# Performance work log

Measured on AMD Instinct MI355X. Metric: run time of the kernel, lower is better.

Reference implementation:

```python
import jax, jax.numpy as jnp
import numpy as np

B, N, S, H = 128, 512, 8, 64
HORIZON = 12


def setup_inputs() -> dict:
    key = jax.random.key(0)
    ks = jax.random.split(key, 24)
    sc = 0.05
    inp = {
        "crowd_obsv": jax.random.normal(ks[0], (B, N, S, 2), jnp.float32),
        "pad_mask": jax.random.bernoulli(ks[1], 0.9, (B, N, N)),
        "neg_hist_mask": jnp.ones((B, N, S, 1), jnp.float32),
        # LSTM params (PyTorch layout, gate order i,f,g,o)
        "Wih": jax.random.normal(ks[2], (4 * H, 2), jnp.float32) * sc,
        "Whh": jax.random.normal(ks[3], (4 * H, H), jnp.float32) * sc,
        "bih": jax.random.normal(ks[4], (4 * H,), jnp.float32) * sc,
        "bhh": jax.random.normal(ks[5], (4 * H,), jnp.float32) * sc,
        # human_encoder: ReLU, Linear, ReLU, Linear, ReLU
        "W_enc1": jax.random.normal(ks[6], (H, H), jnp.float32) * sc,
        "b_enc1": jax.random.normal(ks[7], (H,), jnp.float32) * sc,
        "W_enc2": jax.random.normal(ks[8], (H, H), jnp.float32) * sc,
        "b_enc2": jax.random.normal(ks[9], (H,), jnp.float32) * sc,
        # human_head: Linear, ReLU
        "W_head": jax.random.normal(ks[10], (H, H), jnp.float32) * sc,
        "b_head": jax.random.normal(ks[11], (H,), jnp.float32) * sc,
        "Wq": jax.random.normal(ks[12], (H, H), jnp.float32) * sc,
        "bq": jax.random.normal(ks[13], (H,), jnp.float32) * sc,
        "Wk": jax.random.normal(ks[14], (H, H), jnp.float32) * sc,
        "bk": jax.random.normal(ks[15], (H,), jnp.float32) * sc,
        "Wv": jax.random.normal(ks[16], (H, H), jnp.float32) * sc,
        "bv": jax.random.normal(ks[17], (H,), jnp.float32) * sc,
        # human_forecaster: Linear(2H -> horizon*2)
        "Wf": jax.random.normal(ks[18], (HORIZON * 2, 2 * H), jnp.float32) * sc,
        "bf": jax.random.normal(ks[19], (HORIZON * 2,), jnp.float32) * sc,
    }
    return inp


def _forward(crowd_obsv, pad_mask, neg_hist_mask, Wih, Whh, bih, bhh,
             W_enc1, b_enc1, W_enc2, b_enc2, W_head, b_head,
             Wq, bq, Wk, bk, Wv, bv, Wf, bf):
    b, n, s, _ = crowd_obsv.shape
    h_dim = Whh.shape[1]
    horizon = Wf.shape[0] // 2

    x = (crowd_obsv * neg_hist_mask).reshape(-1, s, 2)  # [M, S, 2]
    m = x.shape[0]

    # --- variable-length masking: find last zero index (x-channel) ---
    zero_mask = (x == 0)                                  # [M, S, 2]
    ar = jnp.arange(s)
    lzi = jnp.max(zero_mask * ar[None, :, None], axis=1)  # [M, 2]
    lzi = jnp.where(zero_mask.any(axis=1), lzi, -1)
    lzi = lzi[:, 0]                                       # [M]
    rows = ar[None, :]
    kill = (rows < lzi[:, None]) & (lzi[:, None] >= 0)    # [M, S]
    x = jnp.where(kill[:, :, None], jnp.zeros((), x.dtype), x)
    length = jnp.maximum((s - 1) - lzi, 1)                # clamp(7 - lzi, min=1)

    # --- packed LSTM via masked scan: state frozen once t >= length ---
    bias = bih + bhh

    def step(carry, inp):
        h, c = carry
        xt, t = inp
        gates = xt @ Wih.T + h @ Whh.T + bias           # [M, 4H]
        i, f, g, o = jnp.split(gates, 4, axis=-1)
        c_new = jax.nn.sigmoid(f) * c + jax.nn.sigmoid(i) * jnp.tanh(g)
        h_new = jax.nn.sigmoid(o) * jnp.tanh(c_new)
        upd = (t < length)[:, None]
        return (jnp.where(upd, h_new, h), jnp.where(upd, c_new, c)), None

    init = (jnp.zeros((m, h_dim), x.dtype), jnp.zeros((m, h_dim), x.dtype))
    (hn, _), _ = jax.lax.scan(step, init, (x.transpose(1, 0, 2), jnp.arange(s)))

    he = hn.reshape(b, n, h_dim)

    # human_encoder + human_head
    h1 = jax.nn.relu(he)
    h1 = jax.nn.relu(h1 @ W_enc1.T + b_enc1)
    h1 = jax.nn.relu(h1 @ W_enc2.T + b_enc2)
    hidden = jax.nn.relu(h1 @ W_head.T + b_head)

    q = hidden @ Wq.T + bq
    k = hidden @ Wk.T + bk
    v = hidden @ Wv.T + bv

    logits = jnp.einsum('bnh,bmh->bnm', q, k)
    logits = jnp.where(pad_mask, logits, jnp.asarray(-999999999999.0, logits.dtype))
    attn = jnp.einsum('bnm,bmh->bnh', jax.nn.softmax(logits, axis=2), v)

    feat = jnp.concatenate([v, attn], axis=-1)            # [B, N, 2H]
    forecast = (feat @ Wf.T + bf).reshape(-1, n, horizon, 2)
    return forecast, feat


def reference(crowd_obsv, pad_mask, neg_hist_mask, Wih, Whh, bih, bhh,
              W_enc1, b_enc1, W_enc2, b_enc2, W_head, b_head,
              Wq, bq, Wk, bk, Wv, bv, Wf, bf):
    return _forward(crowd_obsv, pad_mask, neg_hist_mask, Wih, Whh, bih, bhh,
                    W_enc1, b_enc1, W_enc2, b_enc2, W_head, b_head,
                    Wq, bq, Wk, bk, Wv, bv, Wf, bf)
```

## Files before the change

### kernel.cpp

```cpp
#include <hip/hip_runtime.h>
#include <hip/hip_bf16.h>
#include <stdint.h>

#define B_ 128
#define N_ 512
#define S_ 8
#define H_ 64
#define M_ (B_*N_)
#define L2E 1.442695041f

typedef __attribute__((ext_vector_type(8))) short bf16x8;
typedef __attribute__((ext_vector_type(4))) float f32x4;

__device__ __forceinline__ float exp2f_(float x) { return __builtin_amdgcn_exp2f(x); }
__device__ __forceinline__ float rcpf_(float x)  { return __builtin_amdgcn_rcpf(x); }
__device__ __forceinline__ float sig2(float x)  { return rcpf_(1.f + exp2f_(-x)); }
__device__ __forceinline__ float tanh2(float x) { return 1.f - 2.f*rcpf_(exp2f_(x) + 1.f); }
__device__ __forceinline__ float dot4(float4 a, float4 b) {
  return a.x*b.x + a.y*b.y + a.z*b.z + a.w*b.w;
}
__device__ __forceinline__ unsigned short f2bf(float x) {
  unsigned int u = __float_as_uint(x);
  u += 0x7fffu + ((u >> 16) & 1u);
  return (unsigned short)(u >> 16);
}

__global__ __launch_bounds__(512, 4) void lstm_kernel(
    const float* __restrict__ obs, const float* __restrict__ nhm,
    const float* __restrict__ Wih, const float* __restrict__ Whh,
    const float* __restrict__ bih, const float* __restrict__ bhh,
    unsigned short* __restrict__ he)
{
  __shared__ short    Wfrag[32*512];
  __shared__ short    Wxc[1024];
  __shared__ short    h_s[128*72];
  __shared__ uint32_t x_pk[8][128];
  __shared__ int      len_s[128];

  const int tid  = threadIdx.x;
  const int lane = tid & 63;
  const int wv   = tid >> 6;
  const int w16  = wv * 16;
  const int quad = lane >> 4;
  const int col  = lane & 15;
  const int row0 = blockIdx.x * 128;

  #pragma unroll
  for (int i = 0; i < 4; ++i) {
    int p = i*512 + tid;
    int f = p >> 6, l = p & 63;
    int t16 = f >> 1, s = f & 1;
    int lq = l >> 4, lc = l & 15;
    const float sc = (t16 >= 8 && t16 < 12) ? (2.f*L2E) : L2E;
    const float* src = Whh + (size_t)(t16*16 + lc)*64 + s*32 + lq*8;
    short* dst = Wfrag + f*512 + l*8;
    #pragma unroll
    for (int j = 0; j < 8; ++j) dst[j] = (short)f2bf(src[j] * sc);
  }
  if (tid < 256) {
    int t16 = tid >> 4, cc = tid & 15;
    int n = t16*16 + cc;
    const float sc = (t16 >= 8 && t16 < 12) ? (2.f*L2E) : L2E;
    short* d = Wxc + t16*64 + cc*4;
    d[0] = (short)f2bf(Wih[2*n + 0] * sc);
    d[1] = (short)f2bf(Wih[2*n + 1] * sc);
    d[2] = (short)f2bf((bih[n] + bhh[n]) * sc);
    d[3] = 0;
  }

  #pragma unroll
  for (int i = 0; i < 9; ++i) ((uint32_t*)h_s)[i*512 + tid] = 0u;

  {
    const int grow = row0 + w16 + col;
    float xv0[8], xv1[8];
    int lzi = -1;
    #pragma unroll
    for (int t = 0; t < 8; ++t) {
      float m = nhm[(size_t)grow*8 + t];
      float a = obs[((size_t)grow*8 + t)*2 + 0] * m;
      float b = obs[((size_t)grow*8 + t)*2 + 1] * m;
      xv0[t] = a; xv1[t] = b;
      if (a == 0.f) lzi = t;
    }
    if (quad == 0) {
      #pragma unroll
      for (int t = 0; t < 8; ++t) {
        bool kill = (t < lzi);
        float a = kill ? 0.f : xv0[t];
        float b = kill ? 0.f : xv1[t];
        x_pk[t][w16 + col] = (uint32_t)f2bf(a) | ((uint32_t)f2bf(b) << 16);
      }
      int len = 7 - lzi; if (len < 1) len = 1;
      len_s[w16 + col] = len;
    }
  }
  __syncthreads();

  int lenr[4];
  #pragma unroll
  for (int r = 0; r < 4; ++r) lenr[r] = len_s[w16 + quad*4 + r];

  float c_[16];
  #pragma unroll
  for (int i = 0; i < 16; ++i) c_[i] = 0.f;

  const f32x4 zero4 = {0.f, 0.f, 0.f, 0.f};
  const bool q0 = (quad == 0);

  #pragma unroll 1
  for (int t = 0; t < 8; ++t) {
    uint32_t xw = x_pk[t][w16 + col];
    union { bf16x8 v; uint32_t u[4]; } ax;
    ax.u[0] = q0 ? xw : 0u;
    ax.u[1] = q0 ? 0x00003f80u : 0u;
    ax.u[2] = 0u; ax.u[3] = 0u;

    bf16x8 a0 = *(const bf16x8*)(h_s + (w16 + col)*72 + quad*8);
    bf16x8 a1 = *(const bf16x8*)(h_s + (w16 + col)*72 + 32 + quad*8);

    #pragma unroll
    for (int cc = 0; cc < 4; ++cc) {
      f32x4 acc[4];
      #pragma unroll
      for (int g = 0; g < 4; ++g) {
        const int t16 = g*4 + cc;
        union { bf16x8 v; uint32_t u[4]; } wx;
        uint2 d = *(const uint2*)(Wxc + t16*64 + col*4);
        wx.u[0] = q0 ? d.x : 0u;
        wx.u[1] = q0 ? d.y : 0u;
        wx.u[2] = 0u; wx.u[3] = 0u;
        bf16x8 b0 = *(const bf16x8*)(Wfrag + (t16*2+0)*512 + lane*8);
        bf16x8 b1 = *(const bf16x8*)(Wfrag + (t16*2+1)*512 + lane*8);
        acc[g] = __builtin_amdgcn_mfma_f32_16x16x32_bf16(ax.v, wx.v, zero4, 0, 0, 0);
        acc[g] = __builtin_amdgcn_mfma_f32_16x16x32_bf16(a0, b0, acc[g], 0, 0, 0);
        acc[g] = __builtin_amdgcn_mfma_f32_16x16x32_bf16(a1, b1, acc[g], 0, 0, 0);
      }
      #pragma unroll
      for (int r = 0; r < 4; ++r) {
        if (t < lenr[r]) {
          float gi = acc[0][r];
          float gf = acc[1][r];
          float gg = acc[2][r];
          float go = acc[3][r];
          float cn = sig2(gf)*c_[cc*4+r] + sig2(gi)*tanh2(gg);
          c_[cc*4+r] = cn;
          h_s[(w16 + quad*4 + r)*72 + cc*16 + col] =
              (short)f2bf(sig2(go)*tanh2(cn*(2.f*L2E)));
        }
      }
      __builtin_amdgcn_sched_barrier(0);
    }
  }

  #pragma unroll
  for (int s = 0; s < 2; ++s) {
    int chunk = s*64 + lane;
    int rl = chunk >> 3, c8 = chunk & 7;
    bf16x8 v = *(const bf16x8*)(h_s + (w16 + rl)*72 + c8*8);
    #pragma unroll
    for (int j = 0; j < 8; ++j) {
      short sv = v[j];
      v[j] = (sv & (short)0x8000) ? (short)0 : sv;
    }
    *(bf16x8*)(he + (size_t)(row0 + w16 + rl)*64 + c8*8) = v;
  }
}

__global__ __launch_bounds__(256) void mlp_kernel(
    const unsigned short* __restrict__ he,
    const float* __restrict__ W1, const float* __restrict__ b1,
    const float* __restrict__ W2, const float* __restrict__ b2,
    const float* __restrict__ Wh, const float* __restrict__ bh,
    const float* __restrict__ Wq, const float* __restrict__ bq,
    const float* __restrict__ Wk, const float* __restrict__ bk,
    const float* __restrict__ Wv, const float* __restrict__ bv,
    unsigned short* __restrict__ qb, unsigned short* __restrict__ kb,
    unsigned short* __restrict__ vt, float* __restrict__ feat)
{
  __shared__ short Wm[3][8*512];
  __shared__ float bias_s[6*64];
  __shared__ short Atile[4][16*76];

  const int tid  = threadIdx.x;
  const int lane = tid & 63;
  const int wv   = tid >> 6;
  const int quad = lane >> 4;
  const int col  = lane & 15;
  const int rowb = blockIdx.x*64 + wv*16;

  const float* m1[3] = {W1, W2, Wh};
  const float* m2[3] = {Wq, Wk, Wv};
  auto stage3 = [&](const float* const* mats, float sc0) {
    #pragma unroll
    for (int i = 0; i < 6; ++i) {
      int p = i*256 + tid;
      int m = p >> 9, rem = p & 511;
      int f = rem >> 6, l = rem & 63;
      int nt = f >> 1, s = f & 1;
      int lq = l >> 4, lc = l & 15;
      float sc = (m == 0) ? sc0 : 1.f;
      const float* src = mats[m] + (size_t)(nt*16 + lc)*64 + s*32 + lq*8;
      short* dst = &Wm[m][f*512 + l*8];
      #pragma unroll
      for (int j = 0; j < 8; ++j) dst[j] = (short)f2bf(src[j] * sc);
    }
  };
  stage3(m1, 1.f);
  {
    const float* bs[6] = {b1, b2, bh, bq, bk, bv};
    for (int i = tid; i < 384; i += 256) {
      float sc = ((i >> 6) == 3) ? L2E : 1.f;
      bias_s[i] = bs[i>>6][i & 63] * sc;
    }
  }
  __syncthreads();

  bf16x8 a0 = *(const bf16x8*)(he + (size_t)(rowb + col)*64 + quad*8);
  bf16x8 a1 = *(const bf16x8*)(he + (size_t)(rowb + col)*64 + quad*8 + 32);

  f32x4 acc[4];
  auto runL = [&](int m, int bidx) {
    #pragma unroll
    for (int nt = 0; nt < 4; ++nt) {
      float bb = bias_s[bidx*64 + nt*16 + col];
      acc[nt][0] = bb; acc[nt][1] = bb; acc[nt][2] = bb; acc[nt][3] = bb;
    }
    #pragma unroll
    for (int nt = 0; nt < 4; ++nt) {
      bf16x8 bf0 = *(const bf16x8*)(&Wm[m][(nt*2+0)*512 + lane*8]);
      bf16x8 bf1 = *(const bf16x8*)(&Wm[m][(nt*2+1)*512 + lane*8]);
      acc[nt] = __builtin_amdgcn_mfma_f32_16x16x32_bf16(a0, bf0, acc[nt], 0,0,0);
      acc[nt] = __builtin_amdgcn_mfma_f32_16x16x32_bf16(a1, bf1, acc[nt], 0,0,0);
    }
  };
  auto tileWrite = [&](bool relu) {
    #pragma unroll
    for (int nt = 0; nt < 4; ++nt)
      #pragma unroll
      for (int r = 0; r < 4; ++r) {
        float v = relu ? fmaxf(acc[nt][r], 0.f) : acc[nt][r];
        Atile[wv][(quad*4+r)*76 + ((nt*16+col) ^ (r*16))] = (short)f2bf(v);
      }
  };
  auto tileReadA = [&]() {
    int sw = (col & 3) * 16;
    a0 = *(const bf16x8*)(&Atile[wv][col*76 + ((quad*8     ) ^ sw)]);
    a1 = *(const bf16x8*)(&Atile[wv][col*76 + ((quad*8 + 32) ^ sw)]);
  };
  auto storeBF = [&](unsigned short* dst) {
    #pragma unroll
    for (int s = 0; s < 2; ++s) {
      int chunk = s*64 + lane;
      int r = chunk >> 3, c8 = chunk & 7;
      bf16x8 v = *(const bf16x8*)(&Atile[wv][r*76 + ((c8*8) ^ ((r&3)*16))]);
      *(bf16x8*)(dst + (size_t)(rowb + r)*64 + c8*8) = v;
    }
  };

  runL(0, 0); tileWrite(true); tileReadA();
  runL(1, 1); tileWrite(true); tileReadA();
  runL(2, 2); tileWrite(true); tileReadA();
  __syncthreads();
  stage3(m2, L2E);
  __syncthreads();

  runL(0, 3); tileWrite(false); storeBF(qb);
  runL(1, 4); tileWrite(false); storeBF(kb);
  runL(2, 5);
  {
    const int bi   = rowb >> 9;
    const int key0 = (rowb & 511) + quad*4;
    #pragma unroll
    for (int nt = 0; nt < 4; ++nt) {
      #pragma unroll
      for (int r = 0; r < 4; ++r)
        feat[(size_t)(rowb + quad*4 + r)*128 + nt*16 + col] = acc[nt][r];
      uint32_t lo = (uint32_t)f2bf(acc[nt][0]) | ((uint32_t)f2bf(acc[nt][1]) << 16);
      uint32_t hi = (uint32_t)f2bf(acc[nt][2]) | ((uint32_t)f2bf(acc[nt][3]) << 16);
      uint2 pk; pk.x = lo; pk.y = hi;
      *(uint2*)(vt + ((size_t)bi*64 + nt*16 + col)*512 + key0) = pk;
    }
  }
}

__global__ __launch_bounds__(256) void attn_kernel(
    const unsigned short* __restrict__ qg, const unsigned short* __restrict__ kg,
    const unsigned short* __restrict__ vt,
    const int4* __restrict__ pm4, float* __restrict__ feat)
{
  __shared__ short    Ks[128*72];
  __shared__ short    Vt[64*136];
  __shared__ short    Pl[4][16*32];
  __shared__ uint32_t Ms[4][256];

  const int tid  = threadIdx.x;
  const int lane = tid & 63;
  const int wv   = tid >> 6;
  const int quad = lane >> 4;
  const int col  = lane & 15;

  const int b     = blockIdx.x >> 3;
  const int q0    = (blockIdx.x & 7) * 64;
  const int qbase = b*512 + q0 + wv*16;

  bf16x8 qa[2];
  qa[0] = *(const bf16x8*)(qg + (size_t)(qbase + col)*64 + quad*8);
  qa[1] = *(const bf16x8*)(qg + (size_t)(qbase + col)*64 + quad*8 + 32);

  {
    const int4* pw = pm4 + (size_t)qbase * 128;
    const int sh = (lane & 7) * 4;
    #pragma unroll 8
    for (int k = 0; k < 32; ++k) {
      int4 v = pw[k*64 + lane];
      uint32_t nib = (v.x != 0 ? 1u : 0u)
                   | (v.y != 0 ? 2u : 0u)
                   | (v.z != 0 ? 4u : 0u)
                   | (v.w != 0 ? 8u : 0u);
      uint32_t x = nib << sh;
      x |= __shfl_xor(x, 1);
      x |= __shfl_xor(x, 2);
      x |= __shfl_xor(x, 4);
      if ((lane & 7) == 0)
        Ms[wv][k*8 + (lane >> 3)] = x;
    }
  }

  f32x4 o_acc[4];
  #pragma unroll
  for (int nt = 0; nt < 4; ++nt)
    #pragma unroll
    for (int r = 0; r < 4; ++r) o_acc[nt][r] = 0.f;
  float l_part[4] = {0.f, 0.f, 0.f, 0.f};

  const unsigned short* vtb = vt + (size_t)b*64*512;

  for (int c = 0; c < 4; ++c) {
    __syncthreads();
    {
      const int kb_ = b*512 + c*128;
      #pragma unroll
      for (int i = 0; i < 4; ++i) {
        int p = i*256 + tid;
        int key = p >> 3, c8 = p & 7;
        bf16x8 kv = *(const bf16x8*)(kg + (size_t)(kb_ + key)*64 + c8*8);
        *(bf16x8*)(Ks + key*72 + c8*8) = kv;
      }
      #pragma unroll
      for (int i = 0; i < 4; ++i) {
        int p = i*256 + tid;
        int dim = p >> 4, k8 = p & 15;
        bf16x8 vv = *(const bf16x8*)(vtb + (size_t)dim*512 + c*128 + k8*8);
        *(bf16x8*)(Vt + dim*136 + k8*8) = vv;
      }
    }
    __syncthreads();

    for (int kc = 0; kc < 4; ++kc) {
      #pragma unroll
      for (int t = 0; t < 2; ++t) {
        const int kt = kc*2 + t;
        f32x4 s_acc;
        #pragma unroll
        for (int r = 0; r < 4; ++r) s_acc[r] = 0.f;
        const short* kp = Ks + (kt*16 + col)*72 + quad*8;
        bf16x8 kb0 = *(const bf16x8*)(kp);
        bf16x8 kb1 = *(const bf16x8*)(kp + 32);
        s_acc = __builtin_amdgcn_mfma_f32_16x16x32_bf16(qa[0], kb0, s_acc, 0,0,0);
        s_acc = __builtin_amdgcn_mfma_f32_16x16x32_bf16(qa[1], kb1, s_acc, 0,0,0);
        const int kcol = ((t*16 + col) ^ (quad*8));
        #pragma unroll
        for (int r = 0; r < 4; ++r) {
          uint32_t mw = Ms[wv][(quad*4+r)*16 + c*4 + (kt>>1)];
          float p = ((mw >> ((kt&1)*16 + col)) & 1u)
                      ? exp2f_(fminf(s_acc[r], 43.f)) : 0.f;
          l_part[r] += p;
          Pl[wv][(quad*4+r)*32 + kcol] = (short)f2bf(p);
        }
      }
      bf16x8 pa = *(const bf16x8*)(&Pl[wv][col*32 + ((quad*8) ^ (((col)>>2)*8))]);
      #pragma unroll
      for (int nt = 0; nt < 4; ++nt) {
        bf16x8 vb = *(const bf16x8*)(&Vt[(nt*16+col)*136 + kc*32 + quad*8]);
        o_acc[nt] = __builtin_amdgcn_mfma_f32_16x16x32_bf16(pa, vb, o_acc[nt], 0,0,0);
      }
    }
  }

  float inv[4];
  #pragma unroll
  for (int r = 0; r < 4; ++r) {
    float v = l_part[r];
    v += __shfl_xor(v, 1);
    v += __shfl_xor(v, 2);
    v += __shfl_xor(v, 4);
    v += __shfl_xor(v, 8);
    inv[r] = rcpf_(fmaxf(v, 1e-20f));
  }

  #pragma unroll
  for (int nt = 0; nt < 4; ++nt)
    #pragma unroll
    for (int r = 0; r < 4; ++r)
      feat[(size_t)(qbase + quad*4 + r)*128 + 64 + nt*16 + col] = o_acc[nt][r]*inv[r];
}

__global__ __launch_bounds__(256) void forecast_kernel(
    const float* __restrict__ feat, const float* __restrict__ Wf,
    const float* __restrict__ bf, float* __restrict__ out)
{
  __shared__ short Wfr[8*512];
  __shared__ float bl[32];

  const int tid  = threadIdx.x;
  const int lane = tid & 63;
  const int wv   = tid >> 6;
  const int quad = lane >> 4;
  const int col  = lane & 15;
  const int rowb = blockIdx.x*64 + wv*16;

  #pragma unroll
  for (int i = 0; i < 2; ++i) {
    int p = i*256 + tid;
    int f = p >> 6, l = p & 63;
    int kc = f >> 1, nt = f & 1;
    int lq = l >> 4, lc = l & 15;
    int n = nt*16 + lc;
    bf16x8 v;
    #pragma unroll
    for (int j = 0; j < 8; ++j) v[j] = 0;
    if (n < 24) {
      const float* src = Wf + (size_t)n*128 + kc*32 + lq*8;
      #pragma unroll
      for (int j = 0; j < 8; ++j) v[j] = (short)f2bf(src[j]);
    }
    *(bf16x8*)(Wfr + f*512 + l*8) = v;
  }
  if (tid < 32) bl[tid] = (tid < 24) ? bf[tid] : 0.f;
  __syncthreads();

  bf16x8 af[4];
  const float* fr = feat + (size_t)(rowb + col)*128;
  #pragma unroll
  for (int kc = 0; kc < 4; ++kc) {
    float4 f0 = *(const float4*)(fr + kc*32 + quad*8);
    float4 f1 = *(const float4*)(fr + kc*32 + quad*8 + 4);
    af[kc][0]=(short)f2bf(f0.x); af[kc][1]=(short)f2bf(f0.y);
    af[kc][2]=(short)f2bf(f0.z); af[kc][3]=(short)f2bf(f0.w);
    af[kc][4]=(short)f2bf(f1.x); af[kc][5]=(short)f2bf(f1.y);
    af[kc][6]=(short)f2bf(f1.z); af[kc][7]=(short)f2bf(f1.w);
  }

  f32x4 acc[2];
  #pragma unroll
  for (int nt = 0; nt < 2; ++nt) {
    float bb = bl[nt*16 + col];
    acc[nt][0] = bb; acc[nt][1] = bb; acc[nt][2] = bb; acc[nt][3] = bb;
  }
  #pragma unroll
  for (int kc = 0; kc < 4; ++kc) {
    #pragma unroll
    for (int nt = 0; nt < 2; ++nt) {
      bf16x8 b = *(const bf16x8*)(Wfr + (kc*2+nt)*512 + lane*8);
      acc[nt] = __builtin_amdgcn_mfma_f32_16x16x32_bf16(af[kc], b, acc[nt], 0,0,0);
    }
  }

  #pragma unroll
  for (int nt = 0; nt < 2; ++nt) {
    int n = nt*16 + col;
    if (n < 24) {
      #pragma unroll
      for (int r = 0; r < 4; ++r)
        out[(size_t)(rowb + quad*4 + r)*24 + n] = acc[nt][r];
    }
  }
}

extern "C" void kernel_launch(void* const* d_in, const int* in_sizes, int n_in,
                              void* d_out, int out_size, void* d_ws, size_t ws_size,
                              hipStream_t stream)
{
  const float* obs = (const float*)d_in[0];
  const int*   pm  = (const int*)  d_in[1];
  const float* nhm = (const float*)d_in[2];
  const float* Wih = (const float*)d_in[3];
  const float* Whh = (const float*)d_in[4];
  const float* bih = (const float*)d_in[5];
  const float* bhh = (const float*)d_in[6];
  const float* W1  = (const float*)d_in[7];
  const float* b1  = (const float*)d_in[8];
  const float* W2  = (const float*)d_in[9];
  const float* b2  = (const float*)d_in[10];
  const float* Wh  = (const float*)d_in[11];
  const float* bh  = (const float*)d_in[12];
  const float* Wq  = (const float*)d_in[13];
  const float* bq  = (const float*)d_in[14];
  const float* Wk  = (const float*)d_in[15];
  const float* bk  = (const float*)d_in[16];
  const float* Wv  = (const float*)d_in[17];
  const float* bv  = (const float*)d_in[18];
  const float* Wf  = (const float*)d_in[19];
  const float* bf  = (const float*)d_in[20];

  float* out  = (float*)d_out;
  float* feat = out + (size_t)M_*24;

  char* ws = (char*)d_ws;
  unsigned short* he  = (unsigned short*)(ws);
  unsigned short* qbf = (unsigned short*)(ws + (size_t) 8*1024*1024);
  unsigned short* kbf = (unsigned short*)(ws + (size_t)16*1024*1024);
  unsigned short* vtb = (unsigned short*)(ws + (size_t)24*1024*1024);

  lstm_kernel<<<M_/128, 512, 0, stream>>>(obs, nhm, Wih, Whh, bih, bhh, he);
  mlp_kernel<<<M_/64, 256, 0, stream>>>(he, W1,b1, W2,b2, Wh,bh, Wq,bq, Wk,bk, Wv,bv,
                                        qbf, kbf, vtb, feat);
  attn_kernel<<<M_/64, 256, 0, stream>>>(qbf, kbf, vtb, (const int4*)pm, feat);
  forecast_kernel<<<M_/64, 256, 0, stream>>>(feat, Wf, bf, out);
}
```

Baseline: 358.4 us.

## Pack pad mask into bitmask inside LSTM timestep loop, reuse in attention

Moves the conversion of the pad mask (stored as 32-bit ints) into a per-query bitmask out of the attention kernel and into the LSTM kernel. Each timestep of the LSTM recurrence reads a slice of the mask and writes packed words to a workspace buffer. The goal is to hide the large mask read behind the latency-bound recurrence. The attention kernel then loads only the compact bitmask. The cost is extra memory traffic and registers inside the LSTM loop, plus a new workspace buffer.

```diff
diff --git a/kernel.cpp b/kernel.cpp
--- a/kernel.cpp
+++ b/kernel.cpp
@@ -16,9 +16,6 @@
 __device__ __forceinline__ float rcpf_(float x)  { return __builtin_amdgcn_rcpf(x); }
 __device__ __forceinline__ float sig2(float x)  { return rcpf_(1.f + exp2f_(-x)); }
 __device__ __forceinline__ float tanh2(float x) { return 1.f - 2.f*rcpf_(exp2f_(x) + 1.f); }
-__device__ __forceinline__ float dot4(float4 a, float4 b) {
-  return a.x*b.x + a.y*b.y + a.z*b.z + a.w*b.w;
-}
 __device__ __forceinline__ unsigned short f2bf(float x) {
   unsigned int u = __float_as_uint(x);
   u += 0x7fffu + ((u >> 16) & 1u);
@@ -29,7 +26,8 @@
     const float* __restrict__ obs, const float* __restrict__ nhm,
     const float* __restrict__ Wih, const float* __restrict__ Whh,
     const float* __restrict__ bih, const float* __restrict__ bhh,
-    unsigned short* __restrict__ he)
+    unsigned short* __restrict__ he,
+    const int4* __restrict__ pm4, uint32_t* __restrict__ bm)
 {
   __shared__ short    Wfrag[32*512];
   __shared__ short    Wxc[1024];
@@ -44,6 +42,10 @@
   const int quad = lane >> 4;
   const int col  = lane & 15;
   const int row0 = blockIdx.x * 128;
+
+  const int     wb  = (blockIdx.x*8 + wv) * 256;
+  const int4*   pw  = pm4 + (size_t)wb * 8;
+  const int     shp = (lane & 7) * 4;
 
   #pragma unroll
   for (int i = 0; i < 4; ++i) {
@@ -148,6 +150,30 @@
           h_s[(w16 + quad*4 + r)*72 + cc*16 + col] =
               (short)f2bf(sig2(go)*tanh2(cn*(2.f*L2E)));
         }
+      }
+      __builtin_amdgcn_sched_barrier(0);
+    }
+
+    {
+      const int4* ps = pw + t*256 + lane;
+      int4 v0 = ps[0];
+      int4 v1 = ps[64];
+      int4 v2 = ps[128];
+      int4 v3 = ps[192];
+      int4 vv[4] = {v0, v1, v2, v3};
+      #pragma unroll
+      for (int jj = 0; jj < 4; ++jj) {
+        int4 v = vv[jj];
+        uint32_t nib = (v.x != 0 ? 1u : 0u)
+                     | (v.y != 0 ? 2u : 0u)
+                     | (v.z != 0 ? 4u : 0u)
+                     | (v.w != 0 ? 8u : 0u);
+        uint32_t x = nib << shp;
+        x |= __shfl_xor(x, 1);
+        x |= __shfl_xor(x, 2);
+        x |= __shfl_xor(x, 4);
+        if ((lane & 7) == 0)
+          bm[wb + t*32 + jj*8 + (lane >> 3)] = x;
       }
       __builtin_amdgcn_sched_barrier(0);
     }
@@ -287,7 +313,7 @@
 __global__ __launch_bounds__(256) void attn_kernel(
     const unsigned short* __restrict__ qg, const unsigned short* __restrict__ kg,
     const unsigned short* __restrict__ vt,
-    const int4* __restrict__ pm4, float* __restrict__ feat)
+    const uint32_t* __restrict__ bm, float* __restrict__ feat)
 {
   __shared__ short    Ks[128*72];
   __shared__ short    Vt[64*136];
@@ -308,24 +334,9 @@
   qa[0] = *(const bf16x8*)(qg + (size_t)(qbase + col)*64 + quad*8);
   qa[1] = *(const bf16x8*)(qg + (size_t)(qbase + col)*64 + quad*8 + 32);
 
-  {
-    const int4* pw = pm4 + (size_t)qbase * 128;
-    const int sh = (lane & 7) * 4;
-    #pragma unroll 8
-    for (int k = 0; k < 32; ++k) {
-      int4 v = pw[k*64 + lane];
-      uint32_t nib = (v.x != 0 ? 1u : 0u)
-                   | (v.y != 0 ? 2u : 0u)
-                   | (v.z != 0 ? 4u : 0u)
-                   | (v.w != 0 ? 8u : 0u);
-      uint32_t x = nib << sh;
-      x |= __shfl_xor(x, 1);
-      x |= __shfl_xor(x, 2);
-      x |= __shfl_xor(x, 4);
-      if ((lane & 7) == 0)
-        Ms[wv][k*8 + (lane >> 3)] = x;
-    }
-  }
+  #pragma unroll
+  for (int w = 0; w < 4; ++w)
+    Ms[wv][w*64 + lane] = bm[(size_t)qbase*16 + w*64 + lane];
 
   f32x4 o_acc[4];
   #pragma unroll
@@ -512,10 +523,12 @@
   unsigned short* qbf = (unsigned short*)(ws + (size_t) 8*1024*1024);
   unsigned short* kbf = (unsigned short*)(ws + (size_t)16*1024*1024);
   unsigned short* vtb = (unsigned short*)(ws + (size_t)24*1024*1024);
-
-  lstm_kernel<<<M_/128, 512, 0, stream>>>(obs, nhm, Wih, Whh, bih, bhh, he);
+  uint32_t*       bmw = (uint32_t*)      (ws + (size_t)32*1024*1024);
+
+  lstm_kernel<<<M_/128, 512, 0, stream>>>(obs, nhm, Wih, Whh, bih, bhh, he,
+                                          (const int4*)pm, bmw);
   mlp_kernel<<<M_/64, 256, 0, stream>>>(he, W1,b1, W2,b2, Wh,bh, Wq,bq, Wk,bk, Wv,bv,
                                         qbf, kbf, vtb, feat);
-  attn_kernel<<<M_/64, 256, 0, stream>>>(qbf, kbf, vtb, (const int4*)pm, feat);
+  attn_kernel<<<M_/64, 256, 0, stream>>>(qbf, kbf, vtb, bmw, feat);
   forecast_kernel<<<M_/64, 256, 0, stream>>>(feat, Wf, bf, out);
 }
```

After: 320.3 us. -10.6%, faster.
